# Kernel optimization log

Measured on AMD Instinct MI355X. Metric: run time of the kernel, lower is better.

The kernel has to match this reference:

```python
import jax, jax.numpy as jnp
import numpy as np

# uniform-size batching: B graphs, NC compound atoms, NP pocket residues each
B, NC, NP, H = 16, 64, 384, 128
CFEAT, PFEAT = 56, 1280
SCALE = 5.0  # coordinate_scale
LN_EPS = 1e-5


def setup_inputs() -> dict:
    key = jax.random.key(0)
    ks = jax.random.split(key, 16)
    inp = {
        "compound_feats": jax.random.normal(ks[0], (B * NC, CFEAT), jnp.float32),
        "pocket_feats": jax.random.normal(ks[1], (B * NP, PFEAT), jnp.float32),
        "complex_coords": jax.random.normal(ks[2], (B, 2 + NC + NP, 3), jnp.float32) * 10.0,
        "pocket_xyz": jax.random.normal(ks[3], (B, NP, 3), jnp.float32) * 10.0,
        "dis_map": jax.random.uniform(ks[4], (B * NP * NC,), jnp.float32) * 10.0,
        # learned parameters (xavier with gain=0.001 as in the torch init)
        "Wc": jax.random.normal(ks[5], (CFEAT, H), jnp.float32) * 0.001,
        "bc": jnp.zeros((H,), jnp.float32),
        "Wp": jax.random.normal(ks[6], (PFEAT, H), jnp.float32) * 0.001,
        "bp": jnp.zeros((H,), jnp.float32),
        "ln_g": jnp.ones((H,), jnp.float32),
        "ln_b": jnp.zeros((H,), jnp.float32),
        "W1": jax.random.normal(ks[7], (H, H), jnp.float32) * 0.001,
        "b1": jnp.zeros((H,), jnp.float32),
        "W2": jax.random.normal(ks[8], (H, 1), jnp.float32) * 0.001,
        "b2": jnp.zeros((1,), jnp.float32),
    }
    return inp


def _layernorm(x, g, b):
    m = jnp.mean(x, axis=-1, keepdims=True)
    v = jnp.mean(jnp.square(x - m), axis=-1, keepdims=True)
    return (x - m) * jax.lax.rsqrt(v + LN_EPS) * g + b


def reference(compound_feats, pocket_feats, complex_coords, pocket_xyz, dis_map,
              Wc, bc, Wp, bp, ln_g, ln_b, W1, b1, W2, b2):
    norm = lambda x: x / SCALE
    # input linears, then dense-batch (uniform sizes -> exact reshape)
    comp_emb = (compound_feats @ Wc + bc).reshape(B, NC, H)   # [B,NC,H]
    pock_emb = (pocket_feats @ Wp + bp).reshape(B, NP, H)     # [B,NP,H]
    # complex layout per graph: [glb_c, compound (NC), glb_p, pocket (NP)]
    # complex_binding_model treated as identity (see notes): emb/coords pass through.
    comp_coords_out = norm(complex_coords[:, 1:1 + NC])       # [B,NC,3] (normalized)
    pock_coords = norm(pocket_xyz)                            # [B,NP,3]
    # torch.cdist(pocket, compound): [B,NP,NC]
    diff = pock_coords[:, :, None, :] - comp_coords_out[:, None, :, :]
    pc_dis = jnp.sqrt(jnp.sum(jnp.square(diff), axis=-1))
    # layernorm + pairwise outer product + distmap MLP
    p_ln = _layernorm(pock_emb, ln_g, ln_b)
    c_ln = _layernorm(comp_emb, ln_g, ln_b)
    z = jnp.einsum('bik,bjk->bijk', p_ln, c_ln)               # [B,NP,NC,H]
    h = jax.nn.relu(z @ W1 + b1)
    b_logit = (h @ W2 + b2)[..., 0]                            # [B,NP,NC]
    # uniform sizes -> all-true masks, boolean-select is a flatten
    dis_map_pred_by_pair = jax.nn.sigmoid(b_logit.reshape(-1)) * 10.0
    dis_map_pred_by_coord = jnp.clip(pc_dis.reshape(-1) * SCALE, 0.0, 10.0)
    compound_coord_pred = (comp_coords_out * SCALE).reshape(B * NC, 3)
    compound_batch = jnp.repeat(jnp.arange(B, dtype=jnp.int32), NC)
    return (compound_coord_pred, compound_batch, dis_map_pred_by_pair,
            dis_map_pred_by_coord, dis_map)
```

## Files before the change

kernel.cpp:

```cpp
#include <hip/hip_runtime.h>
#include <hip/hip_bf16.h>

#define BB 16
#define NC 64
#define NP 384
#define HH 128
#define CF 56
#define PFT 1280

typedef float f32x4 __attribute__((ext_vector_type(4)));
typedef __bf16 bf16x8 __attribute__((ext_vector_type(8)));
typedef unsigned short u16x8 __attribute__((ext_vector_type(8)));
typedef unsigned short u16x4 __attribute__((ext_vector_type(4)));

static __device__ __forceinline__ unsigned short f2bfu(float f){
  __bf16 h = (__bf16)f;
  return __builtin_bit_cast(unsigned short, h);
}
static __device__ __forceinline__ float bfu2f(unsigned short u){
  __bf16 h = __builtin_bit_cast(__bf16, u);
  return (float)h;
}

__global__ __launch_bounds__(256) void k_prep(
    const float* __restrict__ cf, const float* __restrict__ Wc,
    const float* __restrict__ bc, const float* __restrict__ lng,
    const float* __restrict__ lnb, const float* __restrict__ Wp,
    const float* __restrict__ W1, const float* __restrict__ cc,
    const float* __restrict__ px, const float* __restrict__ dm,
    unsigned short* __restrict__ c_ln, unsigned short* __restrict__ wpt,
    unsigned short* __restrict__ w1t,
    float* __restrict__ out1, float* __restrict__ out4, float* __restrict__ out5){
  __shared__ unsigned short t[128][72];
  __shared__ float redc[2][2], redc2[2][2];
  int bx = blockIdx.x;
  int tid = threadIdx.x;
  if (bx < 20){
    int k0 = bx*64;
    #pragma unroll
    for (int i=0;i<8;i++){
      int fi = tid + i*256;
      int k  = fi>>5;
      int c4 = (fi&31)*4;
      float4 v = *(const float4*)(Wp + (size_t)(k0+k)*HH + c4);
      t[c4+0][k]=f2bfu(v.x); t[c4+1][k]=f2bfu(v.y);
      t[c4+2][k]=f2bfu(v.z); t[c4+3][k]=f2bfu(v.w);
    }
    __syncthreads();
    #pragma unroll
    for (int i=0;i<4;i++){
      int ci = tid + i*256;
      int col = ci>>3, kb = ci&7;
      u16x8 v = *(const u16x8*)&t[col][kb*8];
      *(u16x8*)(wpt + (size_t)col*PFT + k0 + kb*8) = v;
    }
  } else if (bx < 84){
    int idx = (bx-20)*256+tid;
    int k = idx>>7, m = idx&127;
    w1t[m*HH+k] = f2bfu(W1[idx]);
  } else if (bx < 596){
    int rh = tid>>7, m = tid&127;
    int row = (bx-84)*2 + rh;
    const float* cr = cf + row*CF;
    float acc = bc[m];
    #pragma unroll
    for (int k=0;k<CF;k++) acc += cr[k]*Wc[k*HH+m];
    float s=acc, s2=acc*acc;
    #pragma unroll
    for (int off=1; off<64; off<<=1){ s += __shfl_xor(s,off,64); s2 += __shfl_xor(s2,off,64); }
    int wid = (tid>>6)&1;
    if ((m&63)==0){ redc[rh][wid]=s; redc2[rh][wid]=s2; }
    __syncthreads();
    float S=redc[rh][0]+redc[rh][1], S2=redc2[rh][0]+redc2[rh][1];
    float mean = S*(1.0f/HH);
    float var  = S2*(1.0f/HH) - mean*mean;
    float rs = rsqrtf(var + 1e-5f);
    c_ln[(size_t)row*HH+m] = f2bfu((acc-mean)*rs*lng[m] + lnb[m]);
  } else if (bx < 608){
    int idx = (bx-596)*256+tid;
    if (idx < BB*NC*3){
      int bb = idx/(NC*3), rem = idx%(NC*3);
      float v = cc[(size_t)bb*(2+NC+NP)*3 + 3 + rem];
      out1[idx] = (v/5.0f)*5.0f;
    }
    if (idx < BB*NC) out1[BB*NC*3+idx] = (float)(idx>>6);
  } else {
    int idx = (bx-608)*256+tid;
    int b = idx/(NP*NC), r = idx%(NP*NC), i = r>>6, j = r&63;
    const float* pp = px + ((size_t)b*NP+i)*3;
    const float* cp = cc + (size_t)b*(2+NC+NP)*3 + 3 + (size_t)j*3;
    float dx=pp[0]/5.0f-cp[0]/5.0f;
    float dy=pp[1]/5.0f-cp[1]/5.0f;
    float dz=pp[2]/5.0f-cp[2]/5.0f;
    float d = sqrtf(dx*dx+dy*dy+dz*dz)*5.0f;
    d = fminf(fmaxf(d,0.f),10.f);
    out4[idx]=d;
    out5[idx]=dm[idx];
  }
}

__global__ __launch_bounds__(256) void k_pock(
    const float* __restrict__ pf, const unsigned short* __restrict__ wpt,
    const float* __restrict__ bp, const float* __restrict__ lng,
    const float* __restrict__ lnb, unsigned short* __restrict__ p_ln){
  __shared__ __align__(16) unsigned short sA[2][2][32*64];
  __shared__ __align__(16) unsigned short sB[2][2][HH*64];
  __shared__ float sBp[HH], sG[HH], sBl[HH];
  int tid = threadIdx.x;
  int w = tid>>6, lane = tid&63, q = lane&15, gr = lane>>4;
  int pair = w>>1, rh = w&1;
  int tp = tid & 127;
  int row0 = blockIdx.x*32;
  if (tid < HH){ sBp[tid]=bp[tid]; sG[tid]=lng[tid]; sBl[tid]=lnb[tid]; }
  f32x4 acc[8];
  #pragma unroll
  for (int nt=0;nt<8;nt++) acc[nt]=(f32x4){0.f,0.f,0.f,0.f};
  int khalf0 = pair*640;
  int rowl = rh*16 + q;
  int arow = tp>>2, ak4 = (tp&3)*16;
  float4 ra[4]; u16x8 rb[8];
  #define LOADS(KS) {                                                        \
    int kbase = khalf0 + (KS)*64;                                            \
    _Pragma("unroll")                                                        \
    for (int i=0;i<4;i++)                                                    \
      ra[i] = *(const float4*)(pf + (size_t)(row0+arow)*PFT + kbase + ak4 + i*4); \
    _Pragma("unroll")                                                        \
    for (int i=0;i<8;i++){                                                   \
      int bi = tp + 128*i;                                                   \
      int col = bi>>3, kb = bi&7;                                            \
      rb[i] = *(const u16x8*)(wpt + (size_t)col*PFT + kbase + kb*8);         \
    }                                                                        \
  }
  #define WRITES(BUF) {                                                      \
    char* A = (char*)&sA[pair][BUF][0];                                      \
    char* Bc = (char*)&sB[pair][BUF][0];                                     \
    _Pragma("unroll")                                                        \
    for (int i=0;i<4;i++){                                                   \
      int k4 = ak4 + i*4;                                                    \
      u16x4 h = { f2bfu(ra[i].x), f2bfu(ra[i].y), f2bfu(ra[i].z), f2bfu(ra[i].w) }; \
      *(u16x4*)(A + arow*128 + (((k4>>3)^(arow&7))<<4) + ((k4&7)<<1)) = h;   \
    }                                                                        \
    _Pragma("unroll")                                                        \
    for (int i=0;i<8;i++){                                                   \
      int bi = tp + 128*i;                                                   \
      int col = bi>>3, kb = bi&7;                                            \
      *(u16x8*)(Bc + col*128 + ((kb^(col&7))<<4)) = rb[i];                   \
    }                                                                        \
  }
  LOADS(0)
  WRITES(0)
  int cur = 0;
  for (int ks=0; ks<10; ks++){
    if (ks<9) LOADS(ks+1)
    __syncthreads();
    char* A = (char*)&sA[pair][cur][0];
    char* Bc = (char*)&sB[pair][cur][0];
    #pragma unroll
    for (int kk=0;kk<2;kk++){
      bf16x8 a = *(bf16x8*)(A + rowl*128 + (((kk*4+gr)^(rowl&7))<<4));
      #pragma unroll
      for (int nt=0;nt<8;nt++){
        int col = nt*16+q;
        bf16x8 b = *(bf16x8*)(Bc + col*128 + (((kk*4+gr)^(col&7))<<4));
        acc[nt] = __builtin_amdgcn_mfma_f32_16x16x32_bf16(a,b,acc[nt],0,0,0);
      }
    }
    if (ks<9){ WRITES(cur^1) cur ^= 1; }
  }
  __syncthreads();
  float* comb = (float*)&sB[0][0][0];
  if (pair==1){
    #pragma unroll
    for (int nt=0;nt<8;nt++)
      #pragma unroll
      for (int r=0;r<4;r++)
        comb[(rh*16+gr*4+r)*HH + nt*16+q] = acc[nt][r];
  }
  __syncthreads();
  if (pair==0){
    float v[8][4];
    #pragma unroll
    for (int nt=0;nt<8;nt++){
      float bpv = sBp[nt*16+q];
      #pragma unroll
      for (int r=0;r<4;r++)
        v[nt][r] = acc[nt][r] + comb[(rh*16+gr*4+r)*HH + nt*16+q] + bpv;
    }
    #pragma unroll
    for (int r=0;r<4;r++){
      float s=0.f, s2=0.f;
      #pragma unroll
      for (int nt=0;nt<8;nt++){ s += v[nt][r]; s2 += v[nt][r]*v[nt][r]; }
      s  += __shfl_xor(s,1,64);  s2 += __shfl_xor(s2,1,64);
      s  += __shfl_xor(s,2,64);  s2 += __shfl_xor(s2,2,64);
      s  += __shfl_xor(s,4,64);  s2 += __shfl_xor(s2,4,64);
      s  += __shfl_xor(s,8,64);  s2 += __shfl_xor(s2,8,64);
      float mean = s*(1.0f/HH);
      float var  = s2*(1.0f/HH) - mean*mean;
      float rs   = rsqrtf(var + 1e-5f);
      int row = row0 + rh*16 + gr*4 + r;
      #pragma unroll
      for (int nt=0;nt<8;nt++){
        int col = nt*16+q;
        p_ln[(size_t)row*HH + col] = f2bfu((v[nt][r]-mean)*rs*sG[col] + sBl[col]);
      }
    }
  }
}

__global__ __launch_bounds__(256,2) void k_pair(
    const unsigned short* __restrict__ c_ln, const unsigned short* __restrict__ p_ln,
    const unsigned short* __restrict__ w1t, const float* __restrict__ b1,
    const float* __restrict__ W2, const float* __restrict__ b2p,
    float* __restrict__ out3){
  __shared__ __align__(16) unsigned short sP[12*HH];
  int tid = threadIdx.x;
  int w = tid>>6, lane = tid&63, q = lane&15, gr = lane>>4;
  int bx = blockIdx.x;
  int b  = bx>>5;
  int i0 = (bx&31)*12;
  {
    const u16x8* src = (const u16x8*)(p_ln + (size_t)(b*NP+i0)*HH);
    for (int c=tid; c<12*HH/8; c+=256) ((u16x8*)sP)[c] = src[c];
  }
  float cf[4][8];
  {
    const unsigned short* cb = c_ln + (size_t)b*NC*HH + (size_t)(w*16+q)*HH + gr*8;
    #pragma unroll
    for (int kt=0;kt<4;kt++){
      u16x8 v = *(const u16x8*)(cb + kt*32);
      #pragma unroll
      for (int e=0;e<8;e++) cf[kt][e] = bfu2f(v[e]);
    }
  }
  bf16x8 w1f[4][8];
  #pragma unroll
  for (int kt=0;kt<4;kt++)
    #pragma unroll
    for (int nt=0;nt<8;nt++)
      w1f[kt][nt] = *(const bf16x8*)(w1t + (size_t)(nt*16+q)*HH + kt*32 + gr*8);
  float b1v[8], w2v[8];
  #pragma unroll
  for (int nt=0;nt<8;nt++){ b1v[nt]=b1[nt*16+q]; w2v[nt]=W2[nt*16+q]; }
  float b2 = b2p[0];
  __syncthreads();
  for (int ii=0; ii<12; ii++){
    f32x4 acc[8];
    #pragma unroll
    for (int nt=0;nt<8;nt++) acc[nt]=(f32x4){0.f,0.f,0.f,0.f};
    #pragma unroll
    for (int kt=0;kt<4;kt++){
      u16x8 pv = *(const u16x8*)&sP[ii*HH + kt*32 + gr*8];
      bf16x8 a;
      #pragma unroll
      for (int e=0;e<8;e++) a[e] = (__bf16)(cf[kt][e]*bfu2f(pv[e]));
      #pragma unroll
      for (int nt=0;nt<8;nt++)
        acc[nt] = __builtin_amdgcn_mfma_f32_16x16x32_bf16(a, w1f[kt][nt], acc[nt], 0,0,0);
    }
    float part[4]={0.f,0.f,0.f,0.f};
    #pragma unroll
    for (int nt=0;nt<8;nt++)
      #pragma unroll
      for (int r=0;r<4;r++){
        float h = acc[nt][r] + b1v[nt];
        h = fmaxf(h, 0.f);
        part[r] += h*w2v[nt];
      }
    #pragma unroll
    for (int r=0;r<4;r++){
      part[r]+=__shfl_xor(part[r],1,16);
      part[r]+=__shfl_xor(part[r],2,16);
      part[r]+=__shfl_xor(part[r],4,16);
      part[r]+=__shfl_xor(part[r],8,16);
    }
    if (q==0){
      float4 o;
      o.x = 10.f/(1.f+expf(-(part[0]+b2)));
      o.y = 10.f/(1.f+expf(-(part[1]+b2)));
      o.z = 10.f/(1.f+expf(-(part[2]+b2)));
      o.w = 10.f/(1.f+expf(-(part[3]+b2)));
      *(float4*)(out3 + (size_t)(b*NP+i0+ii)*NC + w*16 + gr*4) = o;
    }
  }
}

extern "C" void kernel_launch(void* const* d_in, const int* in_sizes, int n_in,
                              void* d_out, int out_size, void* d_ws, size_t ws_size,
                              hipStream_t stream){
  const float* cf = (const float*)d_in[0];
  const float* pf = (const float*)d_in[1];
  const float* cc = (const float*)d_in[2];
  const float* px = (const float*)d_in[3];
  const float* dm = (const float*)d_in[4];
  const float* Wc = (const float*)d_in[5];
  const float* bc = (const float*)d_in[6];
  const float* Wp = (const float*)d_in[7];
  const float* bp = (const float*)d_in[8];
  const float* lng= (const float*)d_in[9];
  const float* lnb= (const float*)d_in[10];
  const float* W1 = (const float*)d_in[11];
  const float* b1 = (const float*)d_in[12];
  const float* W2 = (const float*)d_in[13];
  const float* b2 = (const float*)d_in[14];

  float* out = (float*)d_out;
  char* ws = (char*)d_ws;
  unsigned short* c_ln = (unsigned short*)ws;
  unsigned short* p_ln = (unsigned short*)(ws + 262144);
  unsigned short* w1t  = (unsigned short*)(ws + 262144 + 1572864);
  unsigned short* wpt  = (unsigned short*)(ws + 262144 + 1572864 + 32768);

  float* out1 = out;
  float* out3 = out + BB*NC*3 + BB*NC;
  float* out4 = out3 + BB*NP*NC;
  float* out5 = out4 + BB*NP*NC;

  hipLaunchKernelGGL(k_prep, dim3(2144), dim3(256), 0, stream,
                     cf, Wc, bc, lng, lnb, Wp, W1, cc, px, dm,
                     c_ln, wpt, w1t, out1, out4, out5);
  hipLaunchKernelGGL(k_pock, dim3(BB*NP/32), dim3(256), 0, stream,
                     pf, wpt, bp, lng, lnb, p_ln);
  hipLaunchKernelGGL(k_pair, dim3(512), dim3(256), 0, stream,
                     c_ln, p_ln, w1t, b1, W2, b2, out3);
}
```

Before: 48.26 us.

## Fuse pocket projection and layernorm into the pair MLP kernel

Merges the pocket linear+layernorm kernel into the pairwise MLP kernel. Each of 512 blocks computes its own 12 pocket rows (padded to 16) over the full K=1280 and keeps the fp32 layernorm result in shared memory. This removes a kernel launch and the bf16 p_ln round trip through global memory. In exchange, every block streams the full 320KB Wp transposed weight, so weight traffic grows about 16x (mostly L2 hits). The MFMA tiles also waste a quarter of their rows on padding.

Measured after the change: 44.67 us. -7.4%, faster.

```diff
diff --git a/kernel.cpp b/kernel.cpp
--- a/kernel.cpp
+++ b/kernel.cpp
@@ -99,138 +99,92 @@
   }
 }
 
-__global__ __launch_bounds__(256) void k_pock(
+__global__ __launch_bounds__(256,2) void k_main(
     const float* __restrict__ pf, const unsigned short* __restrict__ wpt,
     const float* __restrict__ bp, const float* __restrict__ lng,
-    const float* __restrict__ lnb, unsigned short* __restrict__ p_ln){
-  __shared__ __align__(16) unsigned short sA[2][2][32*64];
-  __shared__ __align__(16) unsigned short sB[2][2][HH*64];
-  __shared__ float sBp[HH], sG[HH], sBl[HH];
-  int tid = threadIdx.x;
-  int w = tid>>6, lane = tid&63, q = lane&15, gr = lane>>4;
-  int pair = w>>1, rh = w&1;
-  int tp = tid & 127;
-  int row0 = blockIdx.x*32;
-  if (tid < HH){ sBp[tid]=bp[tid]; sG[tid]=lng[tid]; sBl[tid]=lnb[tid]; }
-  f32x4 acc[8];
-  #pragma unroll
-  for (int nt=0;nt<8;nt++) acc[nt]=(f32x4){0.f,0.f,0.f,0.f};
-  int khalf0 = pair*640;
-  int rowl = rh*16 + q;
-  int arow = tp>>2, ak4 = (tp&3)*16;
-  float4 ra[4]; u16x8 rb[8];
-  #define LOADS(KS) {                                                        \
-    int kbase = khalf0 + (KS)*64;                                            \
-    _Pragma("unroll")                                                        \
-    for (int i=0;i<4;i++)                                                    \
-      ra[i] = *(const float4*)(pf + (size_t)(row0+arow)*PFT + kbase + ak4 + i*4); \
-    _Pragma("unroll")                                                        \
-    for (int i=0;i<8;i++){                                                   \
-      int bi = tp + 128*i;                                                   \
-      int col = bi>>3, kb = bi&7;                                            \
-      rb[i] = *(const u16x8*)(wpt + (size_t)col*PFT + kbase + kb*8);         \
-    }                                                                        \
-  }
-  #define WRITES(BUF) {                                                      \
-    char* A = (char*)&sA[pair][BUF][0];                                      \
-    char* Bc = (char*)&sB[pair][BUF][0];                                     \
-    _Pragma("unroll")                                                        \
-    for (int i=0;i<4;i++){                                                   \
-      int k4 = ak4 + i*4;                                                    \
-      u16x4 h = { f2bfu(ra[i].x), f2bfu(ra[i].y), f2bfu(ra[i].z), f2bfu(ra[i].w) }; \
-      *(u16x4*)(A + arow*128 + (((k4>>3)^(arow&7))<<4) + ((k4&7)<<1)) = h;   \
-    }                                                                        \
-    _Pragma("unroll")                                                        \
-    for (int i=0;i<8;i++){                                                   \
-      int bi = tp + 128*i;                                                   \
-      int col = bi>>3, kb = bi&7;                                            \
-      *(u16x8*)(Bc + col*128 + ((kb^(col&7))<<4)) = rb[i];                   \
-    }                                                                        \
-  }
-  LOADS(0)
-  WRITES(0)
-  int cur = 0;
-  for (int ks=0; ks<10; ks++){
-    if (ks<9) LOADS(ks+1)
-    __syncthreads();
-    char* A = (char*)&sA[pair][cur][0];
-    char* Bc = (char*)&sB[pair][cur][0];
-    #pragma unroll
-    for (int kk=0;kk<2;kk++){
-      bf16x8 a = *(bf16x8*)(A + rowl*128 + (((kk*4+gr)^(rowl&7))<<4));
-      #pragma unroll
-      for (int nt=0;nt<8;nt++){
-        int col = nt*16+q;
-        bf16x8 b = *(bf16x8*)(Bc + col*128 + (((kk*4+gr)^(col&7))<<4));
-        acc[nt] = __builtin_amdgcn_mfma_f32_16x16x32_bf16(a,b,acc[nt],0,0,0);
-      }
-    }
-    if (ks<9){ WRITES(cur^1) cur ^= 1; }
-  }
-  __syncthreads();
-  float* comb = (float*)&sB[0][0][0];
-  if (pair==1){
-    #pragma unroll
-    for (int nt=0;nt<8;nt++)
-      #pragma unroll
-      for (int r=0;r<4;r++)
-        comb[(rh*16+gr*4+r)*HH + nt*16+q] = acc[nt][r];
-  }
-  __syncthreads();
-  if (pair==0){
-    float v[8][4];
-    #pragma unroll
-    for (int nt=0;nt<8;nt++){
-      float bpv = sBp[nt*16+q];
-      #pragma unroll
-      for (int r=0;r<4;r++)
-        v[nt][r] = acc[nt][r] + comb[(rh*16+gr*4+r)*HH + nt*16+q] + bpv;
-    }
-    #pragma unroll
-    for (int r=0;r<4;r++){
-      float s=0.f, s2=0.f;
-      #pragma unroll
-      for (int nt=0;nt<8;nt++){ s += v[nt][r]; s2 += v[nt][r]*v[nt][r]; }
-      s  += __shfl_xor(s,1,64);  s2 += __shfl_xor(s2,1,64);
-      s  += __shfl_xor(s,2,64);  s2 += __shfl_xor(s2,2,64);
-      s  += __shfl_xor(s,4,64);  s2 += __shfl_xor(s2,4,64);
-      s  += __shfl_xor(s,8,64);  s2 += __shfl_xor(s2,8,64);
-      float mean = s*(1.0f/HH);
-      float var  = s2*(1.0f/HH) - mean*mean;
-      float rs   = rsqrtf(var + 1e-5f);
-      int row = row0 + rh*16 + gr*4 + r;
-      #pragma unroll
-      for (int nt=0;nt<8;nt++){
-        int col = nt*16+q;
-        p_ln[(size_t)row*HH + col] = f2bfu((v[nt][r]-mean)*rs*sG[col] + sBl[col]);
-      }
-    }
-  }
-}
-
-__global__ __launch_bounds__(256,2) void k_pair(
-    const unsigned short* __restrict__ c_ln, const unsigned short* __restrict__ p_ln,
-    const unsigned short* __restrict__ w1t, const float* __restrict__ b1,
-    const float* __restrict__ W2, const float* __restrict__ b2p,
-    float* __restrict__ out3){
-  __shared__ __align__(16) unsigned short sP[12*HH];
+    const float* __restrict__ lnb,
+    const unsigned short* __restrict__ c_ln, const unsigned short* __restrict__ w1t,
+    const float* __restrict__ b1, const float* __restrict__ W2,
+    const float* __restrict__ b2p, float* __restrict__ out3){
+  __shared__ __align__(16) unsigned short sA[2][16*64];
+  __shared__ __align__(16) unsigned short sB[2][HH*64];
+  __shared__ __align__(16) float sPf[12*HH];
   int tid = threadIdx.x;
   int w = tid>>6, lane = tid&63, q = lane&15, gr = lane>>4;
   int bx = blockIdx.x;
   int b  = bx>>5;
   int i0 = (bx&31)*12;
-  {
-    const u16x8* src = (const u16x8*)(p_ln + (size_t)(b*NP+i0)*HH);
-    for (int c=tid; c<12*HH/8; c+=256) ((u16x8*)sP)[c] = src[c];
-  }
-  float cf[4][8];
+  size_t prow0 = (size_t)(b*NP + i0);
+  *(unsigned short*)((char*)&sA[0][0] + 1536 + tid*2) = 0;
+  *(unsigned short*)((char*)&sA[1][0] + 1536 + tid*2) = 0;
+  f32x4 acc2[2];
+  acc2[0]=(f32x4){0.f,0.f,0.f,0.f}; acc2[1]=(f32x4){0.f,0.f,0.f,0.f};
+  int arow = tid>>4, ak4 = (tid&15)*4;
+  float4 ra; u16x8 rb[4];
+  #define LOADS1(KS) {                                                         \
+    int kbase = (KS)*64;                                                       \
+    if (arow < 12)                                                             \
+      ra = *(const float4*)(pf + (prow0+arow)*PFT + kbase + ak4);              \
+    _Pragma("unroll")                                                          \
+    for (int i=0;i<4;i++){                                                     \
+      int bi = tid + 256*i;                                                    \
+      int col = bi>>3, kb = bi&7;                                              \
+      rb[i] = *(const u16x8*)(wpt + (size_t)col*PFT + kbase + kb*8);           \
+    }                                                                          \
+  }
+  #define WRITES1(BUF) {                                                       \
+    char* A = (char*)&sA[BUF][0];                                              \
+    char* Bc = (char*)&sB[BUF][0];                                             \
+    if (arow < 12){                                                            \
+      u16x4 h = { f2bfu(ra.x), f2bfu(ra.y), f2bfu(ra.z), f2bfu(ra.w) };        \
+      *(u16x4*)(A + arow*128 + (((ak4>>3)^(arow&7))<<4) + ((ak4&7)<<1)) = h;   \
+    }                                                                          \
+    _Pragma("unroll")                                                          \
+    for (int i=0;i<4;i++){                                                     \
+      int bi = tid + 256*i;                                                    \
+      int col = bi>>3, kb = bi&7;                                              \
+      *(u16x8*)(Bc + col*128 + ((kb^(col&7))<<4)) = rb[i];                     \
+    }                                                                          \
+  }
+  LOADS1(0)
+  WRITES1(0)
+  int cur = 0;
+  for (int ks=0; ks<20; ks++){
+    if (ks<19) LOADS1(ks+1)
+    __syncthreads();
+    char* A = (char*)&sA[cur][0];
+    char* Bc = (char*)&sB[cur][0];
+    #pragma unroll
+    for (int kk=0;kk<2;kk++){
+      bf16x8 a = *(bf16x8*)(A + q*128 + (((kk*4+gr)^(q&7))<<4));
+      #pragma unroll
+      for (int ct=0;ct<2;ct++){
+        int col = w*32 + ct*16 + q;
+        bf16x8 bfr = *(bf16x8*)(Bc + col*128 + (((kk*4+gr)^(col&7))<<4));
+        acc2[ct] = __builtin_amdgcn_mfma_f32_16x16x32_bf16(a,bfr,acc2[ct],0,0,0);
+      }
+    }
+    if (ks<19){ WRITES1(cur^1) cur ^= 1; }
+  }
+  __syncthreads();
+  #pragma unroll
+  for (int ct=0;ct<2;ct++){
+    int col = w*32 + ct*16 + q;
+    float bpv = bp[col];
+    #pragma unroll
+    for (int r=0;r<4;r++){
+      int row = gr*4+r;
+      if (row < 12) sPf[row*HH + col] = acc2[ct][r] + bpv;
+    }
+  }
+  float cfr[4][8];
   {
     const unsigned short* cb = c_ln + (size_t)b*NC*HH + (size_t)(w*16+q)*HH + gr*8;
     #pragma unroll
     for (int kt=0;kt<4;kt++){
       u16x8 v = *(const u16x8*)(cb + kt*32);
       #pragma unroll
-      for (int e=0;e<8;e++) cf[kt][e] = bfu2f(v[e]);
+      for (int e=0;e<8;e++) cfr[kt][e] = bfu2f(v[e]);
     }
   }
   bf16x8 w1f[4][8];
@@ -244,16 +198,37 @@
   for (int nt=0;nt<8;nt++){ b1v[nt]=b1[nt*16+q]; w2v[nt]=W2[nt*16+q]; }
   float b2 = b2p[0];
   __syncthreads();
+  {
+    float g0 = lng[lane], g1 = lng[lane+64];
+    float B0 = lnb[lane], B1 = lnb[lane+64];
+    #pragma unroll
+    for (int rr=0; rr<3; rr++){
+      int row = w*3+rr;
+      float a0 = sPf[row*HH + lane], a1 = sPf[row*HH + lane + 64];
+      float s = a0+a1, s2 = a0*a0 + a1*a1;
+      #pragma unroll
+      for (int off=1; off<64; off<<=1){ s += __shfl_xor(s,off,64); s2 += __shfl_xor(s2,off,64); }
+      float mean = s*(1.0f/HH);
+      float var  = s2*(1.0f/HH) - mean*mean;
+      float rs   = rsqrtf(var + 1e-5f);
+      sPf[row*HH + lane]      = (a0-mean)*rs*g0 + B0;
+      sPf[row*HH + lane + 64] = (a1-mean)*rs*g1 + B1;
+    }
+  }
+  __syncthreads();
   for (int ii=0; ii<12; ii++){
     f32x4 acc[8];
     #pragma unroll
     for (int nt=0;nt<8;nt++) acc[nt]=(f32x4){0.f,0.f,0.f,0.f};
     #pragma unroll
     for (int kt=0;kt<4;kt++){
-      u16x8 pv = *(const u16x8*)&sP[ii*HH + kt*32 + gr*8];
+      f32x4 p0 = *(const f32x4*)&sPf[ii*HH + kt*32 + gr*8];
+      f32x4 p1 = *(const f32x4*)&sPf[ii*HH + kt*32 + gr*8 + 4];
       bf16x8 a;
       #pragma unroll
-      for (int e=0;e<8;e++) a[e] = (__bf16)(cf[kt][e]*bfu2f(pv[e]));
+      for (int e=0;e<4;e++) a[e]   = (__bf16)(cfr[kt][e]*p0[e]);
+      #pragma unroll
+      for (int e=0;e<4;e++) a[e+4] = (__bf16)(cfr[kt][e+4]*p1[e]);
       #pragma unroll
       for (int nt=0;nt<8;nt++)
         acc[nt] = __builtin_amdgcn_mfma_f32_16x16x32_bf16(a, w1f[kt][nt], acc[nt], 0,0,0);
@@ -280,7 +255,7 @@
       o.y = 10.f/(1.f+expf(-(part[1]+b2)));
       o.z = 10.f/(1.f+expf(-(part[2]+b2)));
       o.w = 10.f/(1.f+expf(-(part[3]+b2)));
-      *(float4*)(out3 + (size_t)(b*NP+i0+ii)*NC + w*16 + gr*4) = o;
+      *(float4*)(out3 + (prow0+ii)*NC + w*16 + gr*4) = o;
     }
   }
 }
@@ -307,7 +282,6 @@
   float* out = (float*)d_out;
   char* ws = (char*)d_ws;
   unsigned short* c_ln = (unsigned short*)ws;
-  unsigned short* p_ln = (unsigned short*)(ws + 262144);
   unsigned short* w1t  = (unsigned short*)(ws + 262144 + 1572864);
   unsigned short* wpt  = (unsigned short*)(ws + 262144 + 1572864 + 32768);
 
@@ -319,8 +293,6 @@
   hipLaunchKernelGGL(k_prep, dim3(2144), dim3(256), 0, stream,
                      cf, Wc, bc, lng, lnb, Wp, W1, cc, px, dm,
                      c_ln, wpt, w1t, out1, out4, out5);
-  hipLaunchKernelGGL(k_pock, dim3(BB*NP/32), dim3(256), 0, stream,
-                     pf, wpt, bp, lng, lnb, p_ln);
-  hipLaunchKernelGGL(k_pair, dim3(512), dim3(256), 0, stream,
-                     c_ln, p_ln, w1t, b1, W2, b2, out3);
-}
+  hipLaunchKernelGGL(k_main, dim3(512), dim3(256), 0, stream,
+                     pf, wpt, bp, lng, lnb, c_ln, w1t, b1, W2, b2, out3);
+}
```

## Stage W1 in swizzled LDS for pair kernel and halve rows per block

Applied to the files above, without the earlier changes.

The pair kernel stops holding all W1 fragments in registers and instead loads the whole 128x128 bf16 W1 into LDS with an XOR swizzle, reading B fragments from LDS inside the MFMA loop. Compound fragments stay packed as bf16, and pocket rows are converted to fp32 once into LDS. Rows per block drop from 12 to 6, so the grid doubles to 1024 blocks. The aim is to cut register pressure and raise occupancy and parallelism, at the cost of more LDS traffic per MFMA and repeating the 32 KB W1 load in every block. The renaming of the k_pock macros is cosmetic.

Measured after the change: 45.04 us. -6.7%, faster.

```diff
diff --git a/kernel.cpp b/kernel.cpp
--- a/kernel.cpp
+++ b/kernel.cpp
@@ -119,39 +119,39 @@
   int rowl = rh*16 + q;
   int arow = tp>>2, ak4 = (tp&3)*16;
   float4 ra[4]; u16x8 rb[8];
-  #define LOADS(KS) {                                                        \
-    int kbase = khalf0 + (KS)*64;                                            \
-    _Pragma("unroll")                                                        \
-    for (int i=0;i<4;i++)                                                    \
+  #define LOADSP(KS) {                                                        \
+    int kbase = khalf0 + (KS)*64;                                             \
+    _Pragma("unroll")                                                         \
+    for (int i=0;i<4;i++)                                                     \
       ra[i] = *(const float4*)(pf + (size_t)(row0+arow)*PFT + kbase + ak4 + i*4); \
-    _Pragma("unroll")                                                        \
-    for (int i=0;i<8;i++){                                                   \
-      int bi = tp + 128*i;                                                   \
-      int col = bi>>3, kb = bi&7;                                            \
-      rb[i] = *(const u16x8*)(wpt + (size_t)col*PFT + kbase + kb*8);         \
-    }                                                                        \
-  }
-  #define WRITES(BUF) {                                                      \
-    char* A = (char*)&sA[pair][BUF][0];                                      \
-    char* Bc = (char*)&sB[pair][BUF][0];                                     \
-    _Pragma("unroll")                                                        \
-    for (int i=0;i<4;i++){                                                   \
-      int k4 = ak4 + i*4;                                                    \
+    _Pragma("unroll")                                                         \
+    for (int i=0;i<8;i++){                                                    \
+      int bi = tp + 128*i;                                                    \
+      int col = bi>>3, kb = bi&7;                                             \
+      rb[i] = *(const u16x8*)(wpt + (size_t)col*PFT + kbase + kb*8);          \
+    }                                                                         \
+  }
+  #define WRITESP(BUF) {                                                      \
+    char* A = (char*)&sA[pair][BUF][0];                                       \
+    char* Bc = (char*)&sB[pair][BUF][0];                                      \
+    _Pragma("unroll")                                                         \
+    for (int i=0;i<4;i++){                                                    \
+      int k4 = ak4 + i*4;                                                     \
       u16x4 h = { f2bfu(ra[i].x), f2bfu(ra[i].y), f2bfu(ra[i].z), f2bfu(ra[i].w) }; \
-      *(u16x4*)(A + arow*128 + (((k4>>3)^(arow&7))<<4) + ((k4&7)<<1)) = h;   \
-    }                                                                        \
-    _Pragma("unroll")                                                        \
-    for (int i=0;i<8;i++){                                                   \
-      int bi = tp + 128*i;                                                   \
-      int col = bi>>3, kb = bi&7;                                            \
-      *(u16x8*)(Bc + col*128 + ((kb^(col&7))<<4)) = rb[i];                   \
-    }                                                                        \
-  }
-  LOADS(0)
-  WRITES(0)
+      *(u16x4*)(A + arow*128 + (((k4>>3)^(arow&7))<<4) + ((k4&7)<<1)) = h;    \
+    }                                                                         \
+    _Pragma("unroll")                                                         \
+    for (int i=0;i<8;i++){                                                    \
+      int bi = tp + 128*i;                                                    \
+      int col = bi>>3, kb = bi&7;                                             \
+      *(u16x8*)(Bc + col*128 + ((kb^(col&7))<<4)) = rb[i];                    \
+    }                                                                         \
+  }
+  LOADSP(0)
+  WRITESP(0)
   int cur = 0;
   for (int ks=0; ks<10; ks++){
-    if (ks<9) LOADS(ks+1)
+    if (ks<9) LOADSP(ks+1)
     __syncthreads();
     char* A = (char*)&sA[pair][cur][0];
     char* Bc = (char*)&sB[pair][cur][0];
@@ -165,7 +165,7 @@
         acc[nt] = __builtin_amdgcn_mfma_f32_16x16x32_bf16(a,b,acc[nt],0,0,0);
       }
     }
-    if (ks<9){ WRITES(cur^1) cur ^= 1; }
+    if (ks<9){ WRITESP(cur^1) cur ^= 1; }
   }
   __syncthreads();
   float* comb = (float*)&sB[0][0][0];
@@ -208,55 +208,66 @@
   }
 }
 
-__global__ __launch_bounds__(256,2) void k_pair(
+__global__ __launch_bounds__(256) void k_pair(
     const unsigned short* __restrict__ c_ln, const unsigned short* __restrict__ p_ln,
     const unsigned short* __restrict__ w1t, const float* __restrict__ b1,
     const float* __restrict__ W2, const float* __restrict__ b2p,
     float* __restrict__ out3){
-  __shared__ __align__(16) unsigned short sP[12*HH];
+  __shared__ __align__(16) unsigned short sW[HH*HH];
+  __shared__ __align__(16) float sPf[6*HH];
   int tid = threadIdx.x;
   int w = tid>>6, lane = tid&63, q = lane&15, gr = lane>>4;
   int bx = blockIdx.x;
-  int b  = bx>>5;
-  int i0 = (bx&31)*12;
+  int b  = bx>>6;
+  int i0 = (bx&63)*6;
+  size_t prow0 = (size_t)(b*NP + i0);
   {
-    const u16x8* src = (const u16x8*)(p_ln + (size_t)(b*NP+i0)*HH);
-    for (int c=tid; c<12*HH/8; c+=256) ((u16x8*)sP)[c] = src[c];
-  }
-  float cf[4][8];
+    const int4* srcW = (const int4*)w1t;
+    #pragma unroll
+    for (int i=0;i<8;i++){
+      int c = tid + 256*i;
+      int mm = c>>4, kb = c&15;
+      ((int4*)sW)[mm*16 + (kb^(mm&7))] = srcW[c];
+    }
+  }
+  if (tid < 96){
+    int row = tid>>4, off = (tid&15)*8;
+    u16x8 v = *(const u16x8*)(p_ln + (prow0+row)*HH + off);
+    #pragma unroll
+    for (int e=0;e<8;e++) sPf[row*HH + off + e] = bfu2f(v[e]);
+  }
+  u16x8 cfrag[4];
   {
     const unsigned short* cb = c_ln + (size_t)b*NC*HH + (size_t)(w*16+q)*HH + gr*8;
     #pragma unroll
-    for (int kt=0;kt<4;kt++){
-      u16x8 v = *(const u16x8*)(cb + kt*32);
-      #pragma unroll
-      for (int e=0;e<8;e++) cf[kt][e] = bfu2f(v[e]);
-    }
-  }
-  bf16x8 w1f[4][8];
-  #pragma unroll
-  for (int kt=0;kt<4;kt++)
-    #pragma unroll
-    for (int nt=0;nt<8;nt++)
-      w1f[kt][nt] = *(const bf16x8*)(w1t + (size_t)(nt*16+q)*HH + kt*32 + gr*8);
+    for (int kt=0;kt<4;kt++) cfrag[kt] = *(const u16x8*)(cb + kt*32);
+  }
   float b1v[8], w2v[8];
   #pragma unroll
   for (int nt=0;nt<8;nt++){ b1v[nt]=b1[nt*16+q]; w2v[nt]=W2[nt*16+q]; }
   float b2 = b2p[0];
   __syncthreads();
-  for (int ii=0; ii<12; ii++){
+  for (int ii=0; ii<6; ii++){
     f32x4 acc[8];
     #pragma unroll
     for (int nt=0;nt<8;nt++) acc[nt]=(f32x4){0.f,0.f,0.f,0.f};
     #pragma unroll
     for (int kt=0;kt<4;kt++){
-      u16x8 pv = *(const u16x8*)&sP[ii*HH + kt*32 + gr*8];
+      int kblk = kt*4+gr;
+      f32x4 p0 = *(const f32x4*)&sPf[ii*HH + kblk*8];
+      f32x4 p1 = *(const f32x4*)&sPf[ii*HH + kblk*8 + 4];
+      u16x8 cfv = cfrag[kt];
       bf16x8 a;
       #pragma unroll
-      for (int e=0;e<8;e++) a[e] = (__bf16)(cf[kt][e]*bfu2f(pv[e]));
-      #pragma unroll
-      for (int nt=0;nt<8;nt++)
-        acc[nt] = __builtin_amdgcn_mfma_f32_16x16x32_bf16(a, w1f[kt][nt], acc[nt], 0,0,0);
+      for (int e=0;e<4;e++) a[e]   = (__bf16)(bfu2f(cfv[e])*p0[e]);
+      #pragma unroll
+      for (int e=0;e<4;e++) a[e+4] = (__bf16)(bfu2f(cfv[e+4])*p1[e]);
+      #pragma unroll
+      for (int nt=0;nt<8;nt++){
+        int mm = nt*16+q;
+        bf16x8 bv = *(const bf16x8*)&sW[mm*HH + ((kblk^(mm&7))<<3)];
+        acc[nt] = __builtin_amdgcn_mfma_f32_16x16x32_bf16(a, bv, acc[nt], 0,0,0);
+      }
     }
     float part[4]={0.f,0.f,0.f,0.f};
     #pragma unroll
@@ -280,7 +291,7 @@
       o.y = 10.f/(1.f+expf(-(part[1]+b2)));
       o.z = 10.f/(1.f+expf(-(part[2]+b2)));
       o.w = 10.f/(1.f+expf(-(part[3]+b2)));
-      *(float4*)(out3 + (size_t)(b*NP+i0+ii)*NC + w*16 + gr*4) = o;
+      *(float4*)(out3 + (prow0+ii)*NC + w*16 + gr*4) = o;
     }
   }
 }
@@ -321,6 +332,6 @@
                      c_ln, wpt, w1t, out1, out4, out5);
   hipLaunchKernelGGL(k_pock, dim3(BB*NP/32), dim3(256), 0, stream,
                      pf, wpt, bp, lng, lnb, p_ln);
-  hipLaunchKernelGGL(k_pair, dim3(512), dim3(256), 0, stream,
+  hipLaunchKernelGGL(k_pair, dim3(1024), dim3(256), 0, stream,
                      c_ln, p_ln, w1t, b1, W2, b2, out3);
 }
```
